# Performance work log

Measured on AMD Instinct MI355X. Metric: run time of the kernel, lower is better.

Reference implementation:

```python
import jax, jax.numpy as jnp
import numpy as np

N = 100000        # nodes
E = 1600000       # edges (before self loops)
IN_DIM = 128
OUT_DIM = 64
HEADS = 4
CH = OUT_DIM // HEADS   # 16 channels per head
G = 64            # graphs in batch
EPS = 1e-5        # GraphNorm eps
SLOPE = 0.2       # LeakyReLU negative slope (GATv2Conv default)


def setup_inputs() -> dict:
    key = jax.random.key(0)
    ks = jax.random.split(key, 8)
    x = jax.random.normal(ks[0], (N, IN_DIM), dtype=jnp.float32)
    edge_index = jax.random.randint(ks[1], (2, E), 0, N, dtype=jnp.int64)
    batch = jnp.sort(jax.random.randint(ks[2], (N,), 0, G, dtype=jnp.int64))
    s_in = 1.0 / np.sqrt(IN_DIM)
    # GATv2Conv params (share_weights=False): W_l for source, W_r for target
    Wl = jax.random.normal(ks[3], (IN_DIM, HEADS * CH), dtype=jnp.float32) * s_in
    Wr = jax.random.normal(ks[4], (IN_DIM, HEADS * CH), dtype=jnp.float32) * s_in
    att = jax.random.normal(ks[5], (HEADS, CH), dtype=jnp.float32) * (1.0 / np.sqrt(CH))
    conv_bias = jnp.zeros((HEADS * CH,), dtype=jnp.float32)
    # skip Linear
    skip_W = jax.random.normal(ks[6], (IN_DIM, OUT_DIM), dtype=jnp.float32) * s_in
    skip_b = jax.random.normal(ks[7], (OUT_DIM,), dtype=jnp.float32) * s_in
    # GraphNorm params (PyG init: weight=1, bias=0, mean_scale=1)
    ones = jnp.ones((OUT_DIM,), dtype=jnp.float32)
    zeros = jnp.zeros((OUT_DIM,), dtype=jnp.float32)
    return {
        "x": x, "edge_index": edge_index, "batch": batch,
        "Wl": Wl, "Wr": Wr, "att": att, "conv_bias": conv_bias,
        "skip_W": skip_W, "skip_b": skip_b,
        "bn_w": ones, "bn_b": zeros, "bn_ms": ones,
        "sn_w": ones, "sn_b": zeros, "sn_ms": ones,
    }


def _gatv2(x, Wl, Wr, att, bias, src, dst):
    n = x.shape[0]
    xl = (x @ Wl).reshape(n, HEADS, CH)   # source transform (also the message)
    xr = (x @ Wr).reshape(n, HEADS, CH)   # target transform
    # GATv2: score = a . LeakyReLU(xl[j] + xr[i]) per head
    e = jax.nn.leaky_relu(xl[src] + xr[dst], SLOPE)          # [E,H,C]
    score = jnp.einsum('ehc,hc->eh', e, att)                  # [E,H]
    # segment softmax over edges sharing a target node
    smax = jax.ops.segment_max(score, dst, num_segments=n)    # [N,H]
    ex = jnp.exp(score - smax[dst])
    denom = jax.ops.segment_sum(ex, dst, num_segments=n)
    alpha = ex / denom[dst]                                   # [E,H]
    out = jax.ops.segment_sum(xl[src] * alpha[:, :, None], dst, num_segments=n)
    return out.reshape(n, HEADS * CH) + bias


def _graph_norm(x, w, b, ms, batch):
    cnt = jax.ops.segment_sum(jnp.ones((x.shape[0],), x.dtype), batch, num_segments=G)
    cnt = jnp.maximum(cnt, 1.0)[:, None]
    mean = jax.ops.segment_sum(x, batch, num_segments=G) / cnt
    cen = x - mean[batch] * ms
    var = jax.ops.segment_sum(cen * cen, batch, num_segments=G) / cnt
    inv = jax.lax.rsqrt(var + EPS)
    return w * cen * inv[batch] + b


def reference(x, edge_index, batch, Wl, Wr, att, conv_bias, skip_W, skip_b,
              bn_w, bn_b, bn_ms, sn_w, sn_b, sn_ms):
    n = x.shape[0]
    loop = jnp.arange(n, dtype=edge_index.dtype)  # add_self_loops=True default
    src = jnp.concatenate([edge_index[0], loop])
    dst = jnp.concatenate([edge_index[1], loop])
    x_main = _gatv2(x, Wl, Wr, att, conv_bias, src, dst)
    x_main = _graph_norm(x_main, bn_w, bn_b, bn_ms, batch)
    x_skip = _graph_norm(x @ skip_W + skip_b, sn_w, sn_b, sn_ms, batch)
    return jax.nn.elu(x_main + x_skip)
```

## Files before the change

kernel.cpp:

```cpp
#include <hip/hip_runtime.h>

#define IND 128
#define OUTD 64
#define NG 64
#define NPART 8
#define NSTRIPE 256
#define SLOPE 0.2f
#define EPSV 1e-5f
#define JMASK 131071
#define DEGCAP 48
#define NSB (NG * NPART)
#define GSLOT 4

typedef short bf16x8 __attribute__((ext_vector_type(8)));
typedef float f32x4 __attribute__((ext_vector_type(4)));
typedef float f32x2 __attribute__((ext_vector_type(2)));

__device__ __forceinline__ unsigned bf16rne(float f) {
  unsigned u = __float_as_uint(f);
  return (u + 0x7fffu + ((u >> 16) & 1u)) >> 16;
}
__device__ __forceinline__ unsigned pack2(float a, float b) {
  return bf16rne(a) | (bf16rne(b) << 16);
}
__device__ __forceinline__ unsigned pack2u(unsigned a, unsigned b) {
  return pack2(__uint_as_float(a), __uint_as_float(b));
}

__device__ __forceinline__ void gload_lds16(const void* g, void* l) {
  __builtin_amdgcn_global_load_lds(
      (const __attribute__((address_space(1))) void*)g,
      (__attribute__((address_space(3))) void*)l, 16, 0, 2);
}

__global__ __launch_bounds__(256) void wcvt_kernel(
    const float* __restrict__ Wl, const float* __restrict__ Wr,
    const float* __restrict__ Ws, unsigned short* __restrict__ wt) {
  int i = blockIdx.x * 256 + threadIdx.x;
  if (i >= 3 * 64 * 128) return;
  int k = i & 127, col = (i >> 7) & 63, which = i >> 13;
  const float* W = (which == 0) ? Wl : (which == 1) ? Wr : Ws;
  int m = col >> 2;
  int t = which * 4 + (col & 3);
  int kc = k >> 5, quad = (k >> 3) & 3, j = k & 7;
  int slot = ((t * 4 + kc) * 4 + quad) * 16 + m;
  wt[slot * 8 + j] = (unsigned short)bf16rne(W[k * OUTD + col]);
}

__device__ __forceinline__ void gemm3_body(
    int bx, const float* __restrict__ x, const unsigned short* __restrict__ wt,
    const float* __restrict__ skip_b,
    unsigned* __restrict__ xlb, unsigned* __restrict__ xrb,
    unsigned* __restrict__ xsb,
    int n, uint4* ldsx) {
  int tid = threadIdx.x;
  int wave = tid >> 6, lane = tid & 63;
  int m = lane & 15, quad = lane >> 4;

#pragma unroll
  for (int i = 0; i < 8; ++i) {
    int c = i * 256 + tid;
    int row = c >> 5, u = c & 31;
    int us = u ^ (row & 7);
    int growc = min(bx * 64 + row, n - 1);
    gload_lds16(x + (size_t)growc * IND + us * 4, &ldsx[c]);
  }
  __syncthreads();

  int lbase = (wave * 16 + m) * 32;
  int swz = m & 7;
  union { uint4 u; bf16x8 v; } af[4];
#pragma unroll
  for (int kc = 0; kc < 4; ++kc) {
    int u0 = kc * 8 + quad * 2;
    uint4 A0 = ldsx[lbase + (u0 ^ swz)];
    uint4 A1 = ldsx[lbase + ((u0 + 1) ^ swz)];
    af[kc].u = make_uint4(pack2u(A0.x, A0.y), pack2u(A0.z, A0.w),
                          pack2u(A1.x, A1.y), pack2u(A1.z, A1.w));
  }

  f32x4 acc[12] = {};
#pragma unroll
  for (int kc = 0; kc < 4; ++kc) {
#pragma unroll
    for (int t = 0; t < 12; ++t) {
      const bf16x8* bp =
          (const bf16x8*)&wt[(((t * 4 + kc) * 4 + quad) * 16 + m) * 8];
      acc[t] = __builtin_amdgcn_mfma_f32_16x16x32_bf16(af[kc].v, *bp, acc[t], 0, 0, 0);
    }
  }

  f32x4 sb = *(const f32x4*)&skip_b[4 * m];

  int orow_base = bx * 64 + wave * 16 + quad * 4;
#pragma unroll
  for (int r = 0; r < 4; ++r) {
    int orow = orow_base + r;
    bool ok = orow < n;
    int wbase = (orow << 5) + 2 * m;
    if (ok) {
      uint2 vl; vl.x = pack2(acc[0][r], acc[1][r]);
      vl.y = pack2(acc[2][r], acc[3][r]);
      *(uint2*)&xlb[wbase] = vl;
      uint2 vr; vr.x = pack2(acc[4][r], acc[5][r]);
      vr.y = pack2(acc[6][r], acc[7][r]);
      *(uint2*)&xrb[wbase] = vr;
      uint2 vs; vs.x = pack2(acc[8][r] + sb.x, acc[9][r] + sb.y);
      vs.y = pack2(acc[10][r] + sb.z, acc[11][r] + sb.w);
      *(uint2*)&xsb[wbase] = vs;
    }
  }
}

__device__ __forceinline__ void scat1(int d, int s, int lo, int hi,
                                      int* count, int* __restrict__ bucket) {
  if (d >= lo && d < hi) {
    int p = atomicAdd(&count[d], 1);
    if (p < DEGCAP) bucket[d * DEGCAP + p] = s;
  }
}

__device__ __forceinline__ void scatter_body(int r, int stripe,
                                             const int* __restrict__ src,
                                             const int* __restrict__ dst,
                                             int* count, int* __restrict__ bucket,
                                             int E, int n8) {
  int lo = r * n8, hi = lo + n8;
  int per = (((E + NSTRIPE - 1) / NSTRIPE) + 3) & ~3;
  int s0 = stripe * per;
  int s1 = min(E, s0 + per);
  for (int e = s0 + (int)threadIdx.x * 4; e < s1; e += 1024) {
    if (e + 4 <= s1) {
      int4 d4 = *(const int4*)&dst[e];
      int4 s4 = *(const int4*)&src[e];
      scat1(d4.x, s4.x, lo, hi, count, bucket);
      scat1(d4.y, s4.y, lo, hi, count, bucket);
      scat1(d4.z, s4.z, lo, hi, count, bucket);
      scat1(d4.w, s4.w, lo, hi, count, bucket);
    } else {
      for (int q = e; q < s1; ++q)
        scat1(dst[q], src[q], lo, hi, count, bucket);
    }
  }
}

__device__ __forceinline__ void goff_body(int bx, const int* __restrict__ batch,
                                          int* goff, int n) {
  int i = bx * 256 + threadIdx.x;
  if (i >= n) return;
  int b = batch[i];
  int prev = (i == 0) ? -1 : batch[i - 1];
  for (int g = prev + 1; g <= b; ++g) goff[g] = i;
  if (i == n - 1)
    for (int g = b + 1; g <= NG; ++g) goff[g] = n;
}

__global__ __launch_bounds__(256) void mega1_kernel(
    const float* __restrict__ x, const unsigned short* __restrict__ wt,
    const float* __restrict__ skip_b,
    unsigned* __restrict__ xlb, unsigned* __restrict__ xrb,
    unsigned* __restrict__ xsb,
    const int* __restrict__ src, const int* __restrict__ dst,
    int* count, int* bucket,
    const int* __restrict__ batch, int* goff,
    int n, int E, int n8, int nbG, int nbB, int SG, int GG) {
  __shared__ uint4 ldsx[2048];
  int group = blockIdx.x >> 3, pos = blockIdx.x & 7;
  int gtot = SG + GG;
  int before = (int)(((long long)group * SG) / gtot);
  int after  = (int)(((long long)(group + 1) * SG) / gtot);
  if (after > before) {
    scatter_body(pos, before, src, dst, count, bucket, E, n8);
  } else {
    int g = (group - before) * 8 + pos;
    if (g < nbG) gemm3_body(g, x, wt, skip_b, xlb, xrb, xsb, n, ldsx);
    else if (g < nbG + nbB) goff_body(g - nbG, batch, goff, n);
  }
}

__global__ __launch_bounds__(256) void edge_kernel(
    const unsigned* __restrict__ xlb, const unsigned* __restrict__ xrb,
    const int* __restrict__ count, const int* __restrict__ bucket,
    const float* __restrict__ att, const float* __restrict__ conv_bias,
    const unsigned* __restrict__ xsb, const int* __restrict__ goff,
    float* __restrict__ part,
    unsigned* __restrict__ outb, int n) {
  int tid = threadIdx.x;
  int bxr = (int)blockIdx.x;

  if (bxr < NSB) {
    int g = bxr >> 3, q = bxr & 7;
    int start = goff[g], end = goff[g + 1];
    int col = tid & 63, grp = tid >> 6;
    float s1s = 0.f, s2s = 0.f;
    for (int node = start + q * 4 + grp; node < end; node += 4 * NPART) {
      unsigned w2 = __builtin_nontemporal_load(&xsb[(node << 5) | (col >> 1)]);
      float vs = __uint_as_float((col & 1) ? (w2 & 0xffff0000u) : (w2 << 16));
      s1s += vs; s2s += vs * vs;
    }
    __shared__ float red[2][4][64];
    red[0][grp][col] = s1s; red[1][grp][col] = s2s;
    __syncthreads();
    if (tid < 64) {
      float* dstp = &part[(g * NPART + q) * 256 + 128];
#pragma unroll
      for (int st = 0; st < 2; ++st) {
        float s = red[st][0][tid] + red[st][1][tid] + red[st][2][tid] +
                  red[st][3][tid];
        dstp[st * 64 + tid] = s;
      }
    }
    return;
  }

  int bx = bxr - NSB;
  int wave = tid >> 6;
  int lane = tid & 63;
  int half = lane >> 5;
  int sub = lane & 31;
  int node = bx * 8 + wave * 2 + half;
  bool act = node < n;
  int nodec = min(node, n - 1);

  unsigned ur = __builtin_nontemporal_load(&xrb[(nodec << 5) | sub]);
  float xrc0 = __uint_as_float(ur << 16);
  float xrc1 = __uint_as_float(ur & 0xffff0000u);
  unsigned us = xlb[(nodec << 5) | sub];
  float xs0 = __uint_as_float(us << 16);
  float xs1 = __uint_as_float(us & 0xffff0000u);
  float2 att2 = *(const float2*)&att[sub << 1];

  float t0 = xs0 + xrc0, t1 = xs1 + xrc1;
  t0 = fmaxf(t0, SLOPE * t0);
  t1 = fmaxf(t1, SLOPE * t1);
  float s = t0 * att2.x + t1 * att2.y;
  s += __shfl_xor(s, 1);
  s += __shfl_xor(s, 2);
  s += __shfl_xor(s, 4);
  const float sself = s;

  int e0 = nodec * DEGCAP;
  int deg = min(count[nodec], DEGCAP);
  int iters = max(deg, __shfl_xor(deg, 32));

  float denom = 1.f;
  float a0 = xs0, a1 = xs1;
  int i = 0;
  for (; i + 7 < iters; i += 8) {
    float p[8], v0[8], v1[8];
#pragma unroll
    for (int k = 0; k < 8; ++k) {
      bool a = (i + k < deg);
      int e = a ? (e0 + i + k) : e0;
      int j = bucket[e] & JMASK;
      unsigned u = xlb[(j << 5) | sub];
      v0[k] = __uint_as_float(u << 16);
      v1[k] = __uint_as_float(u & 0xffff0000u);
      float tx = v0[k] + xrc0, ty = v1[k] + xrc1;
      tx = fmaxf(tx, SLOPE * tx); ty = fmaxf(ty, SLOPE * ty);
      float sc = tx * att2.x + ty * att2.y;
      sc += __shfl_xor(sc, 1);
      sc += __shfl_xor(sc, 2);
      sc += __shfl_xor(sc, 4);
      p[k] = a ? __expf(sc - sself) : 0.f;
    }
#pragma unroll
    for (int k = 0; k < 8; ++k) {
      denom += p[k];
      a0 += p[k] * v0[k];
      a1 += p[k] * v1[k];
    }
  }
  for (; i < iters; ++i) {
    bool a = (i < deg);
    int e = a ? (e0 + i) : e0;
    int j = bucket[e] & JMASK;
    unsigned u = xlb[(j << 5) | sub];
    float v0 = __uint_as_float(u << 16);
    float v1 = __uint_as_float(u & 0xffff0000u);
    float tx = v0 + xrc0, ty = v1 + xrc1;
    tx = fmaxf(tx, SLOPE * tx); ty = fmaxf(ty, SLOPE * ty);
    float sc = tx * att2.x + ty * att2.y;
    sc += __shfl_xor(sc, 1);
    sc += __shfl_xor(sc, 2);
    sc += __shfl_xor(sc, 4);
    float p = a ? __expf(sc - sself) : 0.f;
    denom += p;
    a0 += p * v0;
    a1 += p * v1;
  }
  float inv = 1.f / denom;
  float2 cb = *(const float2*)&conv_bias[sub << 1];
  if (act) {
    unsigned w2 = pack2(a0 * inv + cb.x, a1 * inv + cb.y);
    __builtin_nontemporal_store(w2, &outb[(nodec << 5) | sub]);
  }
}

__global__ __launch_bounds__(256) void stats_part_kernel(
    const unsigned* __restrict__ outb,
    const int* __restrict__ goff, float* __restrict__ part) {
  int g = blockIdx.x, q = blockIdx.y;
  int start = goff[g], end = goff[g + 1];
  int col = threadIdx.x & 63, grp = threadIdx.x >> 6;
  float s1m = 0.f, s2m = 0.f;
  for (int node = start + q * 4 + grp; node < end; node += 4 * NPART) {
    unsigned w2 = __builtin_nontemporal_load(&outb[(node << 5) | (col >> 1)]);
    float vm = __uint_as_float((col & 1) ? (w2 & 0xffff0000u) : (w2 << 16));
    s1m += vm; s2m += vm * vm;
  }
  __shared__ float red[2][4][64];
  red[0][grp][col] = s1m; red[1][grp][col] = s2m;
  __syncthreads();
  if (threadIdx.x < 64) {
    int c = threadIdx.x;
    float* dst = &part[(g * NPART + q) * 256];
#pragma unroll
    for (int st = 0; st < 2; ++st) {
      float s = red[st][0][c] + red[st][1][c] + red[st][2][c] + red[st][3][c];
      dst[st * 64 + c] = s;
    }
  }
}

__global__ __launch_bounds__(256) void final_kernel(
    const unsigned* __restrict__ xsb, const unsigned* __restrict__ outb,
    const int* __restrict__ batch,
    const float* __restrict__ part, const int* __restrict__ goff,
    const float* __restrict__ bn_w, const float* __restrict__ bn_b,
    const float* __restrict__ bn_ms,
    const float* __restrict__ sn_w, const float* __restrict__ sn_b,
    const float* __restrict__ sn_ms,
    float* out, int n) {
  __shared__ float A1s[GSLOT][64], B1s[GSLOT][64];
  __shared__ float A2s[GSLOT][64], B2s[GSLOT][64];
  int b = blockIdx.x;
  int tid = threadIdx.x;
  int node0 = b * 16;
  int nodeH = min(node0 + 15, n - 1);
  int gL = batch[node0];
  int gH = batch[nodeH];
  int ng = gH - gL + 1;

  int slot = tid >> 6, c = tid & 63;
  if (slot < ng && slot < GSLOT) {
    int g = gL + slot;
    float S1m = 0.f, S2m = 0.f, S1s = 0.f, S2s = 0.f;
    for (int q = 0; q < NPART; ++q) {
      const float* p = &part[(g * NPART + q) * 256];
      S1m += p[c];       S2m += p[64 + c];
      S1s += p[128 + c]; S2s += p[192 + c];
    }
    float cnt = fmaxf((float)(goff[g + 1] - goff[g]), 1.f);
    float meanM = S1m / cnt;
    float aM = meanM * bn_ms[c];
    float varM = S2m / cnt - 2.f * aM * meanM + aM * aM;
    float invM = rsqrtf(varM + EPSV);
    float am = bn_w[c] * invM;
    A1s[slot][c] = am;
    B1s[slot][c] = bn_b[c] - am * aM;
    float meanS = S1s / cnt;
    float aS = meanS * sn_ms[c];
    float varS = S2s / cnt - 2.f * aS * meanS + aS * aS;
    float invS = rsqrtf(varS + EPSV);
    float as_ = sn_w[c] * invS;
    A2s[slot][c] = as_;
    B2s[slot][c] = sn_b[c] - as_ * aS;
  }
  __syncthreads();

  int idx = b * 256 + tid;
  if (idx >= n * 16) return;
  int node = idx >> 4;
  int c4 = (idx & 15) << 2;
  int sl = min(batch[node] - gL, GSLOT - 1);
  uint2 mw = *(const uint2*)&outb[(node << 5) + (c4 >> 1)];
  float mv0 = __uint_as_float(mw.x << 16);
  float mv1 = __uint_as_float(mw.x & 0xffff0000u);
  float mv2 = __uint_as_float(mw.y << 16);
  float mv3 = __uint_as_float(mw.y & 0xffff0000u);
  uint2 sw = *(const uint2*)&xsb[(node << 5) + (c4 >> 1)];
  float sv0 = __uint_as_float(sw.x << 16);
  float sv1 = __uint_as_float(sw.x & 0xffff0000u);
  float sv2 = __uint_as_float(sw.y << 16);
  float sv3 = __uint_as_float(sw.y & 0xffff0000u);
  f32x4 v;
  v.x = A1s[sl][c4 + 0] * mv0 + B1s[sl][c4 + 0] + A2s[sl][c4 + 0] * sv0 + B2s[sl][c4 + 0];
  v.y = A1s[sl][c4 + 1] * mv1 + B1s[sl][c4 + 1] + A2s[sl][c4 + 1] * sv1 + B2s[sl][c4 + 1];
  v.z = A1s[sl][c4 + 2] * mv2 + B1s[sl][c4 + 2] + A2s[sl][c4 + 2] * sv2 + B2s[sl][c4 + 2];
  v.w = A1s[sl][c4 + 3] * mv3 + B1s[sl][c4 + 3] + A2s[sl][c4 + 3] * sv3 + B2s[sl][c4 + 3];
  v.x = (v.x > 0.f) ? v.x : (__expf(v.x) - 1.f);
  v.y = (v.y > 0.f) ? v.y : (__expf(v.y) - 1.f);
  v.z = (v.z > 0.f) ? v.z : (__expf(v.z) - 1.f);
  v.w = (v.w > 0.f) ? v.w : (__expf(v.w) - 1.f);
  __builtin_nontemporal_store(v, (f32x4*)&out[idx << 2]);
}

extern "C" void kernel_launch(void* const* d_in, const int* in_sizes, int n_in,
                              void* d_out, int out_size, void* d_ws, size_t ws_size,
                              hipStream_t stream) {
  const float* x        = (const float*)d_in[0];
  const int*   ei       = (const int*)d_in[1];
  const int*   batch    = (const int*)d_in[2];
  const float* Wl       = (const float*)d_in[3];
  const float* Wr       = (const float*)d_in[4];
  const float* att      = (const float*)d_in[5];
  const float* conv_b   = (const float*)d_in[6];
  const float* skip_W   = (const float*)d_in[7];
  const float* skip_b   = (const float*)d_in[8];
  const float* bn_w     = (const float*)d_in[9];
  const float* bn_b     = (const float*)d_in[10];
  const float* bn_ms    = (const float*)d_in[11];
  const float* sn_w     = (const float*)d_in[12];
  const float* sn_b     = (const float*)d_in[13];
  const float* sn_ms    = (const float*)d_in[14];

  int n = in_sizes[0] / IND;
  int E = in_sizes[1] / 2;
  const int* src = ei;
  const int* dst = ei + E;
  float* out = (float*)d_out;

  char* w = (char*)d_ws;
  int* count  = (int*)w;   w += (size_t)(n + 64) * 4;
  int* goff   = (int*)w;   w += (size_t)(NG + 64) * 4;
  float* part = (float*)w; w += (size_t)NG * NPART * 256 * 4;
  unsigned short* wt = (unsigned short*)w; w += (size_t)3 * 64 * IND * 2;
  int* bucket = (int*)w;   w += (size_t)n * DEGCAP * 4;
  unsigned* xlb = (unsigned*)w; w += (size_t)n * 32 * 4;
  unsigned* xrb = (unsigned*)w; w += (size_t)n * 32 * 4;
  unsigned* xsb = (unsigned*)w; w += (size_t)n * 32 * 4;
  unsigned* outb = (unsigned*)w; w += (size_t)n * 32 * 4;

  int n8 = (n + 7) / 8;
  int nbG = (n + 63) / 64;
  int nbB = (n + 255) / 256;
  int SG = NSTRIPE;
  int GG = (nbG + nbB + 7) / 8;

  (void)hipMemsetAsync(count, 0, (size_t)(n + 1) * 4, stream);

  wcvt_kernel<<<(3 * 64 * IND + 255) / 256, 256, 0, stream>>>(Wl, Wr, skip_W, wt);

  mega1_kernel<<<8 * (SG + GG), 256, 0, stream>>>(
      x, wt, skip_b, xlb, xrb, xsb, src, dst, count, bucket, batch, goff,
      n, E, n8, nbG, nbB, SG, GG);

  edge_kernel<<<NSB + (n + 7) / 8, 256, 0, stream>>>(
      xlb, xrb, count, bucket, att, conv_b, xsb, goff, part, outb, n);

  dim3 sg(NG, NPART);
  stats_part_kernel<<<sg, 256, 0, stream>>>(outb, goff, part);
  final_kernel<<<(n * 16 + 255) / 256, 256, 0, stream>>>(
      xsb, outb, batch, part, goff, bn_w, bn_b, bn_ms, sn_w, sn_b, sn_ms,
      out, n);
}
```

Measured before the change: 314.3 us.

## Process four nodes per wave with 16 lanes each and 8-byte gathers

```diff
diff --git a/kernel.cpp b/kernel.cpp
--- a/kernel.cpp
+++ b/kernel.cpp
@@ -15,6 +15,7 @@
 typedef short bf16x8 __attribute__((ext_vector_type(8)));
 typedef float f32x4 __attribute__((ext_vector_type(4)));
 typedef float f32x2 __attribute__((ext_vector_type(2)));
+typedef unsigned u32x2 __attribute__((ext_vector_type(2)));
 
 __device__ __forceinline__ unsigned bf16rne(float f) {
   unsigned u = __float_as_uint(f);
@@ -99,15 +100,15 @@
     bool ok = orow < n;
     int wbase = (orow << 5) + 2 * m;
     if (ok) {
-      uint2 vl; vl.x = pack2(acc[0][r], acc[1][r]);
+      u32x2 vl; vl.x = pack2(acc[0][r], acc[1][r]);
       vl.y = pack2(acc[2][r], acc[3][r]);
-      *(uint2*)&xlb[wbase] = vl;
-      uint2 vr; vr.x = pack2(acc[4][r], acc[5][r]);
+      *(u32x2*)&xlb[wbase] = vl;
+      u32x2 vr; vr.x = pack2(acc[4][r], acc[5][r]);
       vr.y = pack2(acc[6][r], acc[7][r]);
-      *(uint2*)&xrb[wbase] = vr;
-      uint2 vs; vs.x = pack2(acc[8][r] + sb.x, acc[9][r] + sb.y);
+      *(u32x2*)&xrb[wbase] = vr;
+      u32x2 vs; vs.x = pack2(acc[8][r] + sb.x, acc[9][r] + sb.y);
       vs.y = pack2(acc[10][r] + sb.z, acc[11][r] + sb.w);
-      *(uint2*)&xsb[wbase] = vs;
+      *(u32x2*)&xsb[wbase] = vs;
     }
   }
 }
@@ -216,84 +217,94 @@
   int bx = bxr - NSB;
   int wave = tid >> 6;
   int lane = tid & 63;
-  int half = lane >> 5;
-  int sub = lane & 31;
-  int node = bx * 8 + wave * 2 + half;
+  int grp = lane >> 4;
+  int s16 = lane & 15;
+  int node = bx * 16 + wave * 4 + grp;
   bool act = node < n;
   int nodec = min(node, n - 1);
-
-  unsigned ur = __builtin_nontemporal_load(&xrb[(nodec << 5) | sub]);
-  float xrc0 = __uint_as_float(ur << 16);
-  float xrc1 = __uint_as_float(ur & 0xffff0000u);
-  unsigned us = xlb[(nodec << 5) | sub];
-  float xs0 = __uint_as_float(us << 16);
-  float xs1 = __uint_as_float(us & 0xffff0000u);
-  float2 att2 = *(const float2*)&att[sub << 1];
-
-  float t0 = xs0 + xrc0, t1 = xs1 + xrc1;
-  t0 = fmaxf(t0, SLOPE * t0);
-  t1 = fmaxf(t1, SLOPE * t1);
-  float s = t0 * att2.x + t1 * att2.y;
+  int wbase = (nodec << 5) + 2 * s16;
+
+  u32x2 rw = *(const u32x2*)&xrb[wbase];
+  float xr0 = __uint_as_float(rw.x << 16);
+  float xr1 = __uint_as_float(rw.x & 0xffff0000u);
+  float xr2 = __uint_as_float(rw.y << 16);
+  float xr3 = __uint_as_float(rw.y & 0xffff0000u);
+  u32x2 lw = *(const u32x2*)&xlb[wbase];
+  float xl0 = __uint_as_float(lw.x << 16);
+  float xl1 = __uint_as_float(lw.x & 0xffff0000u);
+  float xl2 = __uint_as_float(lw.y << 16);
+  float xl3 = __uint_as_float(lw.y & 0xffff0000u);
+  f32x4 at = *(const f32x4*)&att[s16 << 2];
+
+  float t0 = xl0 + xr0, t1 = xl1 + xr1, t2 = xl2 + xr2, t3 = xl3 + xr3;
+  t0 = fmaxf(t0, SLOPE * t0); t1 = fmaxf(t1, SLOPE * t1);
+  t2 = fmaxf(t2, SLOPE * t2); t3 = fmaxf(t3, SLOPE * t3);
+  float s = t0 * at.x + t1 * at.y + t2 * at.z + t3 * at.w;
   s += __shfl_xor(s, 1);
   s += __shfl_xor(s, 2);
-  s += __shfl_xor(s, 4);
   const float sself = s;
 
   int e0 = nodec * DEGCAP;
   int deg = min(count[nodec], DEGCAP);
-  int iters = max(deg, __shfl_xor(deg, 32));
 
   float denom = 1.f;
-  float a0 = xs0, a1 = xs1;
+  float a0 = xl0, a1 = xl1, a2 = xl2, a3 = xl3;
   int i = 0;
-  for (; i + 7 < iters; i += 8) {
-    float p[8], v0[8], v1[8];
+  for (; i + 7 < deg; i += 8) {
+    float p[8], v0[8], v1[8], v2[8], v3[8];
 #pragma unroll
     for (int k = 0; k < 8; ++k) {
-      bool a = (i + k < deg);
-      int e = a ? (e0 + i + k) : e0;
-      int j = bucket[e] & JMASK;
-      unsigned u = xlb[(j << 5) | sub];
-      v0[k] = __uint_as_float(u << 16);
-      v1[k] = __uint_as_float(u & 0xffff0000u);
-      float tx = v0[k] + xrc0, ty = v1[k] + xrc1;
-      tx = fmaxf(tx, SLOPE * tx); ty = fmaxf(ty, SLOPE * ty);
-      float sc = tx * att2.x + ty * att2.y;
+      int j = bucket[e0 + i + k] & JMASK;
+      u32x2 u = *(const u32x2*)&xlb[(j << 5) + 2 * s16];
+      v0[k] = __uint_as_float(u.x << 16);
+      v1[k] = __uint_as_float(u.x & 0xffff0000u);
+      v2[k] = __uint_as_float(u.y << 16);
+      v3[k] = __uint_as_float(u.y & 0xffff0000u);
+      float w0 = v0[k] + xr0, w1 = v1[k] + xr1;
+      float w2 = v2[k] + xr2, w3 = v3[k] + xr3;
+      w0 = fmaxf(w0, SLOPE * w0); w1 = fmaxf(w1, SLOPE * w1);
+      w2 = fmaxf(w2, SLOPE * w2); w3 = fmaxf(w3, SLOPE * w3);
+      float sc = w0 * at.x + w1 * at.y + w2 * at.z + w3 * at.w;
       sc += __shfl_xor(sc, 1);
       sc += __shfl_xor(sc, 2);
-      sc += __shfl_xor(sc, 4);
-      p[k] = a ? __expf(sc - sself) : 0.f;
+      p[k] = __expf(sc - sself);
     }
 #pragma unroll
     for (int k = 0; k < 8; ++k) {
       denom += p[k];
       a0 += p[k] * v0[k];
       a1 += p[k] * v1[k];
-    }
-  }
-  for (; i < iters; ++i) {
-    bool a = (i < deg);
-    int e = a ? (e0 + i) : e0;
-    int j = bucket[e] & JMASK;
-    unsigned u = xlb[(j << 5) | sub];
-    float v0 = __uint_as_float(u << 16);
-    float v1 = __uint_as_float(u & 0xffff0000u);
-    float tx = v0 + xrc0, ty = v1 + xrc1;
-    tx = fmaxf(tx, SLOPE * tx); ty = fmaxf(ty, SLOPE * ty);
-    float sc = tx * att2.x + ty * att2.y;
+      a2 += p[k] * v2[k];
+      a3 += p[k] * v3[k];
+    }
+  }
+  for (; i < deg; ++i) {
+    int j = bucket[e0 + i] & JMASK;
+    u32x2 u = *(const u32x2*)&xlb[(j << 5) + 2 * s16];
+    float v0 = __uint_as_float(u.x << 16);
+    float v1 = __uint_as_float(u.x & 0xffff0000u);
+    float v2 = __uint_as_float(u.y << 16);
+    float v3 = __uint_as_float(u.y & 0xffff0000u);
+    float w0 = v0 + xr0, w1 = v1 + xr1, w2 = v2 + xr2, w3 = v3 + xr3;
+    w0 = fmaxf(w0, SLOPE * w0); w1 = fmaxf(w1, SLOPE * w1);
+    w2 = fmaxf(w2, SLOPE * w2); w3 = fmaxf(w3, SLOPE * w3);
+    float sc = w0 * at.x + w1 * at.y + w2 * at.z + w3 * at.w;
     sc += __shfl_xor(sc, 1);
     sc += __shfl_xor(sc, 2);
-    sc += __shfl_xor(sc, 4);
-    float p = a ? __expf(sc - sself) : 0.f;
+    float p = __expf(sc - sself);
     denom += p;
     a0 += p * v0;
     a1 += p * v1;
+    a2 += p * v2;
+    a3 += p * v3;
   }
   float inv = 1.f / denom;
-  float2 cb = *(const float2*)&conv_bias[sub << 1];
+  f32x4 cb = *(const f32x4*)&conv_bias[s16 << 2];
   if (act) {
-    unsigned w2 = pack2(a0 * inv + cb.x, a1 * inv + cb.y);
-    __builtin_nontemporal_store(w2, &outb[(nodec << 5) | sub]);
+    u32x2 o;
+    o.x = pack2(a0 * inv + cb.x, a1 * inv + cb.y);
+    o.y = pack2(a2 * inv + cb.z, a3 * inv + cb.w);
+    __builtin_nontemporal_store(o, (u32x2*)&outb[wbase]);
   }
 }
 
@@ -374,12 +385,12 @@
   int node = idx >> 4;
   int c4 = (idx & 15) << 2;
   int sl = min(batch[node] - gL, GSLOT - 1);
-  uint2 mw = *(const uint2*)&outb[(node << 5) + (c4 >> 1)];
+  u32x2 mw = *(const u32x2*)&outb[(node << 5) + (c4 >> 1)];
   float mv0 = __uint_as_float(mw.x << 16);
   float mv1 = __uint_as_float(mw.x & 0xffff0000u);
   float mv2 = __uint_as_float(mw.y << 16);
   float mv3 = __uint_as_float(mw.y & 0xffff0000u);
-  uint2 sw = *(const uint2*)&xsb[(node << 5) + (c4 >> 1)];
+  u32x2 sw = *(const u32x2*)&xsb[(node << 5) + (c4 >> 1)];
   float sv0 = __uint_as_float(sw.x << 16);
   float sv1 = __uint_as_float(sw.x & 0xffff0000u);
   float sv2 = __uint_as_float(sw.y << 16);
@@ -446,7 +457,7 @@
       x, wt, skip_b, xlb, xrb, xsb, src, dst, count, bucket, batch, goff,
       n, E, n8, nbG, nbB, SG, GG);
 
-  edge_kernel<<<NSB + (n + 7) / 8, 256, 0, stream>>>(
+  edge_kernel<<<NSB + (n + 15) / 16, 256, 0, stream>>>(
       xlb, xrb, count, bucket, att, conv_b, xsb, goff, part, outb, n);
 
   dim3 sg(NG, NPART);
```

Measured after the change: 328.3 us. 4.4% more time.
